# Kernel optimization log

Hardware: AMD Instinct MI355X
Metric: run time of the kernel (lower is better)

The kernel has to match this reference:

```python
import jax, jax.numpy as jnp
import numpy as np

D_MODEL = 1024
D_K = 64
MAX_LEN = 10000
SCALE = float(np.sqrt(2 * D_K))  # TUPE scale sqrt(2*d_k)


def setup_inputs() -> dict:
    key = jax.random.key(0)
    kq, kk, kv, kpe, kuq, kuk = jax.random.split(key, 6)
    b, s = 4, 2048
    q = jax.random.normal(kq, (b, s, D_MODEL), dtype=jnp.float32)
    k = jax.random.normal(kk, (b, s, D_MODEL), dtype=jnp.float32)
    v = jax.random.normal(kv, (b, s, D_MODEL), dtype=jnp.float32)
    # learned PE, uniform(-0.1, 0.1) as in the source
    pe = jax.random.uniform(kpe, (MAX_LEN, D_MODEL), minval=-0.1, maxval=0.1, dtype=jnp.float32)
    # U_q / U_k: Linear(d_model, d_model, bias=False); store as [in, out] so x @ W matches torch x @ W.T convention after transpose choice
    lim = 1.0 / np.sqrt(D_MODEL)
    Uq = jax.random.uniform(kuq, (D_MODEL, D_MODEL), minval=-lim, maxval=lim, dtype=jnp.float32)
    Uk = jax.random.uniform(kuk, (D_MODEL, D_MODEL), minval=-lim, maxval=lim, dtype=jnp.float32)
    return {"q": q, "k": k, "v": v, "pe": pe, "Uq": Uq, "Uk": Uk}


def reference(q, k, v, pe, Uq, Uk):
    b, len_q, d_model = q.shape
    len_k = k.shape[1]
    # NOTE: source computes scores with FULL q/k (over d_model), not per-head.
    scores = jnp.einsum('bqd,bkd->bqk', q, k)  # [b, lq, lk]
    # TUPE positional attention bias
    q_pe = pe[:len_q] @ Uq  # [lq, d]
    k_pe = pe[:len_k] @ Uk  # [lk, d]
    scores = scores + (q_pe @ k_pe.T)[None, :, :]
    scores = scores / SCALE
    attn = jax.nn.softmax(scores, axis=-1)  # dropout p=0 in eval
    context = jnp.einsum('bqk,bkd->bqd', attn, v)  # [b, lq, d_model]
    # replicate torch transpose(1,2).contiguous().view(b, -1, d_model)
    context = jnp.swapaxes(context, 1, 2).reshape(b, -1, d_model)
    return context, attn
```

## Files before the change

kernel.cpp:

```cpp
#include <hip/hip_runtime.h>
#include <hip/hip_bf16.h>
#include <math.h>

#define BATCH 4
#define SEQ   2048
#define DMODEL 1024

typedef __attribute__((ext_vector_type(8))) short bf16x8;
typedef __attribute__((ext_vector_type(4))) float floatx4;

__device__ __forceinline__ void async_copy16(const void* g, void* lds) {
    __builtin_amdgcn_global_load_lds(
        reinterpret_cast<const unsigned int __attribute__((address_space(1)))*>(
            reinterpret_cast<unsigned long long>(g)),
        reinterpret_cast<unsigned int __attribute__((address_space(3)))*>(
            (unsigned int)reinterpret_cast<unsigned long long>(lds)),
        16, 0, 0);
}

#define SCHED_FENCE() __builtin_amdgcn_sched_barrier(0)


#define T256(T, U, STG, RA, VMM, BARR) do {                                     \
    constexpr int sl = (U) & 3, sl1 = ((U) + 1) & 3, sl3 = ((U) + 3) & 3;       \
    constexpr int p = (U) & 1, p1 = ((U) + 1) & 1;                              \
    _Pragma("unroll") for (int i = 0; i < 4; ++i) aH[i] = readA(sl, 4 + i);     \
    if constexpr (STG) { stageA((T) + 3, 0, sl3); stageA((T) + 3, 1, sl3);      \
                         stageB((T) + 3, 0, sl3); stageB((T) + 3, 1, sl3); }    \
    asm volatile("s_waitcnt lgkmcnt(4)" ::: "memory"); SCHED_FENCE();           \
    __builtin_amdgcn_s_setprio(1);                                              \
    _Pragma("unroll") for (int i = 0; i < 4; ++i)                               \
      _Pragma("unroll") for (int j = 0; j < 4; ++j)                             \
        acc[i][j] = __builtin_amdgcn_mfma_f32_16x16x32_bf16(aP[p][i], bP[p][j], acc[i][j], 0, 0, 0); \
    __builtin_amdgcn_s_setprio(0);                                              \
    if constexpr (RA) {                                                         \
        _Pragma("unroll") for (int i = 0; i < 4; ++i) aP[p1][i] = readA(sl1, i);\
        _Pragma("unroll") for (int j = 0; j < 4; ++j) bP[p1][j] = readB(sl1, j);\
        asm volatile("s_waitcnt lgkmcnt(8)" ::: "memory");                      \
    } else {                                                                    \
        asm volatile("s_waitcnt lgkmcnt(0)" ::: "memory");                      \
    }                                                                           \
    SCHED_FENCE();                                                              \
    __builtin_amdgcn_s_setprio(1);                                              \
    _Pragma("unroll") for (int i = 0; i < 4; ++i)                               \
      _Pragma("unroll") for (int j = 0; j < 4; ++j)                             \
        acc[4 + i][j] = __builtin_amdgcn_mfma_f32_16x16x32_bf16(aH[i], bP[p][j], acc[4 + i][j], 0, 0, 0); \
    __builtin_amdgcn_s_setprio(0);                                              \
    if constexpr ((VMM) == 2)      { asm volatile("s_waitcnt vmcnt(4)" ::: "memory"); } \
    else if constexpr ((VMM) == 1) { asm volatile("s_waitcnt vmcnt(0)" ::: "memory"); } \
    if constexpr (BARR) __builtin_amdgcn_s_barrier();                           \
} while (0)

#define T128(T, U, STG, RA, VMM, BARR) do {                                     \
    constexpr int sl1 = ((U) + 1) & 3, sl3 = ((U) + 3) & 3;                     \
    constexpr int p = (U) & 1, p1 = ((U) + 1) & 1;                              \
    if constexpr (RA) {                                                         \
        _Pragma("unroll") for (int i = 0; i < 8; ++i) aP[p1][i] = readA(sl1, i);\
        _Pragma("unroll") for (int j = 0; j < 2; ++j) bP[p1][j] = readB(sl1, j);\
    }                                                                           \
    if constexpr (STG) { stageA((T) + 3, 0, sl3); stageA((T) + 3, 1, sl3);      \
                         stageB((T) + 3, 0, sl3); }                             \
    if constexpr (RA) { asm volatile("s_waitcnt lgkmcnt(10)" ::: "memory"); }   \
    else              { asm volatile("s_waitcnt lgkmcnt(0)" ::: "memory"); }    \
    SCHED_FENCE();                                                              \
    __builtin_amdgcn_s_setprio(1);                                              \
    _Pragma("unroll") for (int i = 0; i < 8; ++i)                               \
      _Pragma("unroll") for (int j = 0; j < 2; ++j)                             \
        acc[i][j] = __builtin_amdgcn_mfma_f32_16x16x32_bf16(aP[p][i], bP[p][j], acc[i][j], 0, 0, 0); \
    __builtin_amdgcn_s_setprio(0);                                              \
    if constexpr ((VMM) == 2)      { asm volatile("s_waitcnt vmcnt(3)" ::: "memory"); } \
    else if constexpr ((VMM) == 1) { asm volatile("s_waitcnt vmcnt(0)" ::: "memory"); } \
    if constexpr (BARR) __builtin_amdgcn_s_barrier();                           \
} while (0)

template<bool ASPLIT, int BN, bool HAS_BIAS, int MM, int NN, int KK, int KBB>
__global__ __launch_bounds__(512, 1)
void gemm8p(const __hip_bfloat16* __restrict__ A0, const __hip_bfloat16* __restrict__ A1,
            const __hip_bfloat16* __restrict__ B, const float* __restrict__ bias,
            float* __restrict__ C, float scale, long sAb, long sBb, long sCb)
{
    constexpr int BM = 256, BK = 32;
    constexpr int NT = KK / BK;
    constexpr int KA = ASPLIT ? (KK / 2) : KK;
    constexpr int WN = BN / 4, NF = WN / 16;
    constexpr int SLOT_A = BM * BK, SLOT_B = BN * BK;
    constexpr int GX = NN / BN, GY = MM / BM;
    constexpr int CPX = (GX * GY) / 8;
    static_assert(NT % 4 == 0 && NT >= 8, "");
    static_assert((GX * GY) % 8 == 0, "");

    __shared__ __align__(16) __hip_bfloat16 sA[4][SLOT_A];
    __shared__ __align__(16) __hip_bfloat16 sB[4][SLOT_B];

    const int bz = blockIdx.z;
    A0 += (long)bz * sAb;
    if (ASPLIT) A1 += (long)bz * sAb;
    B += (long)bz * sBb;
    C += (long)bz * sCb;

    int b = blockIdx.y * GX + blockIdx.x;
    b = (b & 7) * CPX + (b >> 3);
    const int col0 = (b % GX) * BN;
    const int row0 = (b / GX) * BM;

    const int tid  = threadIdx.x;
    const int wave = tid >> 6, lane = tid & 63;
    const int wm = wave >> 2, wn = wave & 3;
    const int fr = lane & 15, fq = lane >> 4;
    const int swz = (fq ^ ((fr >> 1) & 3)) << 3;

    const int s_r  = (wave << 4) + (lane >> 2);
    const int s_c4 = lane & 3;

    auto stageA = [&](int t, int c, int sl) {
        const int lr = (c << 7) + s_r;
        const int ch = (s_c4 ^ ((lr >> 1) & 3)) << 3;
        int k0 = t << 5;
        const __hip_bfloat16* src = A0;
        if (ASPLIT && k0 >= KA) { src = A1; k0 -= KA; }
        async_copy16(src + (long)(row0 + lr) * KA + k0 + ch,
                     &sA[sl][((c << 7) + (wave << 4)) * BK]);
    };
    auto stageB = [&](int t, int c, int sl) {
        const int lr = (c << 7) + s_r;
        const int ch = (s_c4 ^ ((lr >> 1) & 3)) << 3;
        const int k0 = (t << 5) & (KBB - 1);
        async_copy16(B + (long)(col0 + lr) * KBB + k0 + ch,
                     &sB[sl][((c << 7) + (wave << 4)) * BK]);
    };
    auto readA = [&](int sl, int i) -> bf16x8 {
        return *(const bf16x8*)&sA[sl][((wm << 7) + (i << 4) + fr) * BK + swz];
    };
    auto readB = [&](int sl, int j) -> bf16x8 {
        return *(const bf16x8*)&sB[sl][(wn * WN + (j << 4) + fr) * BK + swz];
    };

    floatx4 acc[8][NF];
    #pragma unroll
    for (int i = 0; i < 8; ++i)
        #pragma unroll
        for (int j = 0; j < NF; ++j) acc[i][j] = (floatx4){0.f, 0.f, 0.f, 0.f};

    bf16x8 aP[2][BN == 256 ? 4 : 8];
    bf16x8 bP[2][NF];
    bf16x8 aH[BN == 256 ? 4 : 1];

    if constexpr (BN == 256) {
        stageA(0, 0, 0); stageA(0, 1, 0); stageB(0, 0, 0); stageB(0, 1, 0);
        stageA(1, 0, 1); stageA(1, 1, 1); stageB(1, 0, 1); stageB(1, 1, 1);
        stageA(2, 0, 2); stageA(2, 1, 2); stageB(2, 0, 2); stageB(2, 1, 2);
        asm volatile("s_waitcnt vmcnt(4)" ::: "memory");
        __builtin_amdgcn_s_barrier(); SCHED_FENCE();
        #pragma unroll
        for (int i = 0; i < 4; ++i) aP[0][i] = readA(0, i);
        #pragma unroll
        for (int j = 0; j < 4; ++j) bP[0][j] = readB(0, j);

        #pragma unroll 1
        for (int tt = 0; tt < NT - 4; tt += 4) {
            T256(tt + 0, 0, 1, 1, 2, 1); T256(tt + 1, 1, 1, 1, 2, 1);
            T256(tt + 2, 2, 1, 1, 2, 1); T256(tt + 3, 3, 1, 1, 2, 1);
        }
        T256(NT - 4, 0, 1, 1, 2, 1);
        T256(NT - 3, 1, 0, 1, 1, 1);
        T256(NT - 2, 2, 0, 1, 0, 0);
        T256(NT - 1, 3, 0, 0, 0, 0);
    } else {
        stageA(0, 0, 0); stageA(0, 1, 0); stageB(0, 0, 0);
        stageA(1, 0, 1); stageA(1, 1, 1); stageB(1, 0, 1);
        stageA(2, 0, 2); stageA(2, 1, 2); stageB(2, 0, 2);
        asm volatile("s_waitcnt vmcnt(3)" ::: "memory");
        __builtin_amdgcn_s_barrier(); SCHED_FENCE();
        #pragma unroll
        for (int i = 0; i < 8; ++i) aP[0][i] = readA(0, i);
        #pragma unroll
        for (int j = 0; j < 2; ++j) bP[0][j] = readB(0, j);

        #pragma unroll 1
        for (int tt = 0; tt < NT - 4; tt += 4) {
            T128(tt + 0, 0, 1, 1, 2, 1); T128(tt + 1, 1, 1, 1, 2, 1);
            T128(tt + 2, 2, 1, 1, 2, 1); T128(tt + 3, 3, 1, 1, 2, 1);
        }
        T128(NT - 4, 0, 1, 1, 2, 1);
        T128(NT - 3, 1, 0, 1, 1, 1);
        T128(NT - 2, 2, 0, 1, 0, 0);
        T128(NT - 1, 3, 0, 0, 0, 0);
    }

    #pragma unroll
    for (int i = 0; i < 8; ++i) {
        #pragma unroll
        for (int r = 0; r < 4; ++r) {
            const int row = row0 + (wm << 7) + (i << 4) + (fq << 2) + r;
            #pragma unroll
            for (int j = 0; j < NF; ++j) {
                const int col = col0 + wn * WN + (j << 4) + fr;
                float val = acc[i][j][r];
                if (HAS_BIAS) val += bias[(long)row * NN + col];
                val *= scale;
                C[(long)row * NN + col] = val;
            }
        }
    }
}

template<bool SPLIT_A, bool HAS_BIAS, bool OUT_TRANS, bool OUT_BF16>
__global__ __launch_bounds__(256, 1)
void mfma_gemm(const __hip_bfloat16* __restrict__ Ah, const __hip_bfloat16* __restrict__ Al,
               const __hip_bfloat16* __restrict__ Bh,
               const float* __restrict__ bias, void* __restrict__ Cvoid,
               int M, int N, int K, float scale,
               long sAb, long sBb, long sCb)
{
    constexpr int NA = SPLIT_A ? 2 : 1;
    __shared__ __align__(16) __hip_bfloat16 sA[NA][128 * 32];
    __shared__ __align__(16) __hip_bfloat16 sB[128 * 32];

    const int bz = blockIdx.z;
    Ah += (long)bz * sAb;
    Bh += (long)bz * sBb;
    if (SPLIT_A) Al += (long)bz * sAb;

    const int row0 = blockIdx.y * 128;
    const int col0 = blockIdx.x * 128;
    const int tid  = threadIdx.x;
    const int wave = tid >> 6;
    const int lane = tid & 63;

    const int srow   = wave * 16 + (lane >> 2);
    const int schunk = (lane & 3) * 8;

    const int wm = (wave >> 1) * 64;
    const int wn = (wave & 1) * 64;
    const int fr = lane & 15;
    const int fk = (lane >> 4) * 8;

    const floatx4 zero = {0.f, 0.f, 0.f, 0.f};
    floatx4 acc[4][4];
    #pragma unroll
    for (int i = 0; i < 4; ++i)
        #pragma unroll
        for (int j = 0; j < 4; ++j) acc[i][j] = zero;

    for (int k0 = 0; k0 < K; k0 += 32) {
        #pragma unroll
        for (int t = 0; t < 2; ++t) {
            const long arow = (long)(row0 + t * 64 + srow);
            const long brow = (long)(col0 + t * 64 + srow);
            const int  soff = (t * 64 + wave * 16) * 32;
            async_copy16(Ah + arow * K + k0 + schunk, &sA[0][soff]);
            async_copy16(Bh + brow * K + k0 + schunk, &sB[soff]);
            if (SPLIT_A)
                async_copy16(Al + arow * K + k0 + schunk, &sA[NA - 1][soff]);
        }
        __syncthreads();

        bf16x8 aH[4], bH[4];
        #pragma unroll
        for (int i = 0; i < 4; ++i) aH[i] = *(const bf16x8*)&sA[0][(wm + i * 16 + fr) * 32 + fk];
        #pragma unroll
        for (int j = 0; j < 4; ++j) bH[j] = *(const bf16x8*)&sB[(wn + j * 16 + fr) * 32 + fk];

        if (SPLIT_A) {
            bf16x8 aL[4];
            #pragma unroll
            for (int i = 0; i < 4; ++i) aL[i] = *(const bf16x8*)&sA[NA - 1][(wm + i * 16 + fr) * 32 + fk];
            #pragma unroll
            for (int i = 0; i < 4; ++i)
                #pragma unroll
                for (int j = 0; j < 4; ++j) {
                    acc[i][j] = __builtin_amdgcn_mfma_f32_16x16x32_bf16(aH[i], bH[j], acc[i][j], 0, 0, 0);
                    acc[i][j] = __builtin_amdgcn_mfma_f32_16x16x32_bf16(aL[i], bH[j], acc[i][j], 0, 0, 0);
                }
        } else {
            #pragma unroll
            for (int i = 0; i < 4; ++i)
                #pragma unroll
                for (int j = 0; j < 4; ++j)
                    acc[i][j] = __builtin_amdgcn_mfma_f32_16x16x32_bf16(aH[i], bH[j], acc[i][j], 0, 0, 0);
        }
        __syncthreads();
    }

    float* Cf = (float*)Cvoid + (long)bz * sCb;
    __hip_bfloat16* Cb = (__hip_bfloat16*)Cvoid + (long)bz * sCb;
    #pragma unroll
    for (int i = 0; i < 4; ++i) {
        #pragma unroll
        for (int r = 0; r < 4; ++r) {
            const int row = row0 + wm + i * 16 + (lane >> 4) * 4 + r;
            #pragma unroll
            for (int j = 0; j < 4; ++j) {
                const int col = col0 + wn + j * 16 + (lane & 15);
                float val = acc[i][j][r];
                if (HAS_BIAS) val += bias[(long)row * N + col];
                val *= scale;
                if (OUT_BF16)       Cb[(long)row * N + col] = __float2bfloat16(val);
                else if (OUT_TRANS) Cf[(long)col * M + row] = val;
                else                Cf[(long)row * N + col] = val;
            }
        }
    }
}

__global__ __launch_bounds__(256)
void convert_bf16_kernel(const float* __restrict__ in, __hip_bfloat16* __restrict__ out, long n)
{
    const long i = ((long)blockIdx.x * 256 + threadIdx.x) * 4;
    if (i >= n) return;
    float va[4];
    *(float4*)va = *(const float4*)(in + i);
    __align__(8) __hip_bfloat16 h[4];
    #pragma unroll
    for (int j = 0; j < 4; ++j) h[j] = __float2bfloat16(va[j]);
    *(uint2*)(out + i) = *(uint2*)h;
}

__global__ __launch_bounds__(256)
void split_convert_kernel(const float* __restrict__ in, __hip_bfloat16* __restrict__ hi,
                          __hip_bfloat16* __restrict__ lo, long n)
{
    const long i = ((long)blockIdx.x * 256 + threadIdx.x) * 4;
    if (i >= n) return;
    float va[4];
    *(float4*)va = *(const float4*)(in + i);
    __align__(8) __hip_bfloat16 h[4], l[4];
    #pragma unroll
    for (int j = 0; j < 4; ++j) {
        h[j] = __float2bfloat16(va[j]);
        l[j] = __float2bfloat16(va[j] - __bfloat162float(h[j]));
    }
    *(uint2*)(hi + i) = *(uint2*)h;
    *(uint2*)(lo + i) = *(uint2*)l;
}

__global__ __launch_bounds__(256)
void transpose_convert_kernel(const float* __restrict__ in, __hip_bfloat16* __restrict__ out,
                              int R, int C, long sIn, long sOut)
{
    in  += (long)blockIdx.z * sIn;
    out += (long)blockIdx.z * sOut;
    __shared__ float t[32][33];
    const int c0 = blockIdx.x * 32, r0 = blockIdx.y * 32;
    for (int i = threadIdx.y; i < 32; i += 8)
        t[i][threadIdx.x] = in[(long)(r0 + i) * C + c0 + threadIdx.x];
    __syncthreads();
    for (int i = threadIdx.y; i < 32; i += 8)
        out[(long)(c0 + i) * R + r0 + threadIdx.x] = __float2bfloat16(t[threadIdx.x][i]);
}

__global__ __launch_bounds__(256)
void softmax_kernel(float* __restrict__ data, __hip_bfloat16* __restrict__ data_bf)
{
    const long row = blockIdx.x;
    float* p = data + row * (long)SEQ;
    __hip_bfloat16* pb = data_bf + row * (long)SEQ;
    const int tid = threadIdx.x;
    const int PER = SEQ / 256;

    float v[PER];
    float m = -1e30f;
    #pragma unroll
    for (int i = 0; i < PER; ++i) {
        v[i] = p[tid + i * 256];
        m = fmaxf(m, v[i]);
    }
    __shared__ float red[256];
    red[tid] = m;
    __syncthreads();
    #pragma unroll
    for (int s = 128; s > 0; s >>= 1) {
        if (tid < s) red[tid] = fmaxf(red[tid], red[tid + s]);
        __syncthreads();
    }
    m = red[0];
    __syncthreads();
    float sum = 0.f;
    #pragma unroll
    for (int i = 0; i < PER; ++i) {
        v[i] = __expf(v[i] - m);
        sum += v[i];
    }
    red[tid] = sum;
    __syncthreads();
    #pragma unroll
    for (int s = 128; s > 0; s >>= 1) {
        if (tid < s) red[tid] += red[tid + s];
        __syncthreads();
    }
    const float inv = 1.0f / red[0];
    #pragma unroll
    for (int i = 0; i < PER; ++i) {
        const float a = v[i] * inv;
        p[tid + i * 256]  = a;
        pb[tid + i * 256] = __float2bfloat16(a);
    }
}

extern "C" void kernel_launch(void* const* d_in, const int* in_sizes, int n_in,
                              void* d_out, int out_size, void* d_ws, size_t ws_size,
                              hipStream_t stream)
{
    const float* q  = (const float*)d_in[0];
    const float* k  = (const float*)d_in[1];
    const float* v  = (const float*)d_in[2];
    const float* pe = (const float*)d_in[3];
    const float* Uq = (const float*)d_in[4];
    const float* Uk = (const float*)d_in[5];

    float* out      = (float*)d_out;
    float* ctx_out  = out;
    float* attn_out = out + (long)BATCH * SEQ * DMODEL;

    const long SD = (long)BATCH * SEQ * DMODEL;
    char* w = (char*)d_ws;
    __hip_bfloat16* q_hi  = (__hip_bfloat16*)w;  w += SD * 2;
    __hip_bfloat16* q_lo  = (__hip_bfloat16*)w;  w += SD * 2;
    __hip_bfloat16* k_bf  = (__hip_bfloat16*)w;  w += SD * 2;
    __hip_bfloat16* pe_bf = (__hip_bfloat16*)w;  w += (long)SEQ * DMODEL * 2;
    __hip_bfloat16* UqT   = (__hip_bfloat16*)w;  w += (long)DMODEL * DMODEL * 2;
    __hip_bfloat16* UkT   = (__hip_bfloat16*)w;  w += (long)DMODEL * DMODEL * 2;
    __hip_bfloat16* qpe_bf= (__hip_bfloat16*)w;  w += (long)SEQ * DMODEL * 2;
    __hip_bfloat16* kpe_bf= (__hip_bfloat16*)w;  w += (long)SEQ * DMODEL * 2;
    float*          biasM = (float*)w;           w += (long)SEQ * SEQ * 4;
    __hip_bfloat16* attn_bf = q_hi;
    __hip_bfloat16* vT      = k_bf;

    const float inv_scale = 1.0f / sqrtf(128.0f);

    convert_bf16_kernel<<<dim3((SEQ * DMODEL) / 4 / 256), 256, 0, stream>>>(pe, pe_bf, (long)SEQ * DMODEL);
    transpose_convert_kernel<<<dim3(DMODEL / 32, DMODEL / 32, 1), dim3(32, 8), 0, stream>>>(
        Uq, UqT, DMODEL, DMODEL, 0, 0);
    transpose_convert_kernel<<<dim3(DMODEL / 32, DMODEL / 32, 1), dim3(32, 8), 0, stream>>>(
        Uk, UkT, DMODEL, DMODEL, 0, 0);
    split_convert_kernel<<<dim3(SD / 4 / 256), 256, 0, stream>>>(q, q_hi, q_lo, SD);
    convert_bf16_kernel<<<dim3(SD / 4 / 256), 256, 0, stream>>>(k, k_bf, SD);

    mfma_gemm<false, false, false, true><<<dim3(DMODEL / 128, SEQ / 128, 2), 256, 0, stream>>>(
        pe_bf, nullptr, UqT, nullptr, qpe_bf, SEQ, DMODEL, DMODEL, 1.0f,
        0, (long)DMODEL * DMODEL, (long)SEQ * DMODEL);

    mfma_gemm<false, false, false, false><<<dim3(SEQ / 128, SEQ / 128, 1), 256, 0, stream>>>(
        qpe_bf, nullptr, kpe_bf, nullptr, biasM, SEQ, SEQ, DMODEL, 1.0f, 0, 0, 0);

    gemm8p<true, 256, true, 2048, 2048, 2048, 1024>
        <<<dim3(SEQ / 256, SEQ / 256, BATCH), 512, 0, stream>>>(
        q_hi, q_lo, k_bf, biasM, attn_out, inv_scale,
        (long)SEQ * DMODEL, (long)SEQ * DMODEL, (long)SEQ * SEQ);

    softmax_kernel<<<dim3(BATCH * SEQ), 256, 0, stream>>>(attn_out, attn_bf);

    transpose_convert_kernel<<<dim3(DMODEL / 32, SEQ / 32, BATCH), dim3(32, 8), 0, stream>>>(
        v, vT, SEQ, DMODEL, (long)SEQ * DMODEL, (long)SEQ * DMODEL);

    gemm8p<false, 128, false, 1024, 2048, 2048, 2048>
        <<<dim3(SEQ / 128, DMODEL / 256, BATCH), 512, 0, stream>>>(
        vT, nullptr, attn_bf, nullptr, ctx_out, 1.0f,
        (long)SEQ * DMODEL, (long)SEQ * SEQ, (long)SEQ * DMODEL);
}
```

Measured before the change: 400.0 us.

## Retile context GEMM to 128x256, reorder staging, use shuffle softmax reductions

The context GEMM switches from a 256x128 tile to a 128x256 tile with a new 4x4 MFMA fragment layout per wave and a matching staging and wait-count schedule. In the 256-tile path, the global-to-LDS staging is moved after the first MFMA batch so it overlaps with compute. The softmax block reduction replaces the LDS tree with its many barriers by wave-level xor shuffles plus a small cross-wave combine. Together these change operand reuse and reduce synchronization, but the altered lgkmcnt/vmcnt waits must still match the new load counts.

```diff
diff --git a/kernel.cpp b/kernel.cpp
--- a/kernel.cpp
+++ b/kernel.cpp
@@ -25,14 +25,14 @@
     constexpr int sl = (U) & 3, sl1 = ((U) + 1) & 3, sl3 = ((U) + 3) & 3;       \
     constexpr int p = (U) & 1, p1 = ((U) + 1) & 1;                              \
     _Pragma("unroll") for (int i = 0; i < 4; ++i) aH[i] = readA(sl, 4 + i);     \
-    if constexpr (STG) { stageA((T) + 3, 0, sl3); stageA((T) + 3, 1, sl3);      \
-                         stageB((T) + 3, 0, sl3); stageB((T) + 3, 1, sl3); }    \
     asm volatile("s_waitcnt lgkmcnt(4)" ::: "memory"); SCHED_FENCE();           \
     __builtin_amdgcn_s_setprio(1);                                              \
     _Pragma("unroll") for (int i = 0; i < 4; ++i)                               \
       _Pragma("unroll") for (int j = 0; j < 4; ++j)                             \
         acc[i][j] = __builtin_amdgcn_mfma_f32_16x16x32_bf16(aP[p][i], bP[p][j], acc[i][j], 0, 0, 0); \
     __builtin_amdgcn_s_setprio(0);                                              \
+    if constexpr (STG) { stageA((T) + 3, 0, sl3); stageA((T) + 3, 1, sl3);      \
+                         stageB((T) + 3, 0, sl3); stageB((T) + 3, 1, sl3); }    \
     if constexpr (RA) {                                                         \
         _Pragma("unroll") for (int i = 0; i < 4; ++i) aP[p1][i] = readA(sl1, i);\
         _Pragma("unroll") for (int j = 0; j < 4; ++j) bP[p1][j] = readB(sl1, j);\
@@ -51,21 +51,21 @@
     if constexpr (BARR) __builtin_amdgcn_s_barrier();                           \
 } while (0)
 
-#define T128(T, U, STG, RA, VMM, BARR) do {                                     \
+#define TCX(T, U, STG, RA, VMM, BARR) do {                                      \
     constexpr int sl1 = ((U) + 1) & 3, sl3 = ((U) + 3) & 3;                     \
     constexpr int p = (U) & 1, p1 = ((U) + 1) & 1;                              \
     if constexpr (RA) {                                                         \
-        _Pragma("unroll") for (int i = 0; i < 8; ++i) aP[p1][i] = readA(sl1, i);\
-        _Pragma("unroll") for (int j = 0; j < 2; ++j) bP[p1][j] = readB(sl1, j);\
+        _Pragma("unroll") for (int i = 0; i < 4; ++i) aP[p1][i] = readA(sl1, i);\
+        _Pragma("unroll") for (int j = 0; j < 4; ++j) bP[p1][j] = readB(sl1, j);\
     }                                                                           \
-    if constexpr (STG) { stageA((T) + 3, 0, sl3); stageA((T) + 3, 1, sl3);      \
-                         stageB((T) + 3, 0, sl3); }                             \
-    if constexpr (RA) { asm volatile("s_waitcnt lgkmcnt(10)" ::: "memory"); }   \
+    if constexpr (STG) { stageA((T) + 3, 0, sl3);                               \
+                         stageB((T) + 3, 0, sl3); stageB((T) + 3, 1, sl3); }    \
+    if constexpr (RA) { asm volatile("s_waitcnt lgkmcnt(8)" ::: "memory"); }    \
     else              { asm volatile("s_waitcnt lgkmcnt(0)" ::: "memory"); }    \
     SCHED_FENCE();                                                              \
     __builtin_amdgcn_s_setprio(1);                                              \
-    _Pragma("unroll") for (int i = 0; i < 8; ++i)                               \
-      _Pragma("unroll") for (int j = 0; j < 2; ++j)                             \
+    _Pragma("unroll") for (int i = 0; i < 4; ++i)                               \
+      _Pragma("unroll") for (int j = 0; j < 4; ++j)                             \
         acc[i][j] = __builtin_amdgcn_mfma_f32_16x16x32_bf16(aP[p][i], bP[p][j], acc[i][j], 0, 0, 0); \
     __builtin_amdgcn_s_setprio(0);                                              \
     if constexpr ((VMM) == 2)      { asm volatile("s_waitcnt vmcnt(3)" ::: "memory"); } \
@@ -73,21 +73,24 @@
     if constexpr (BARR) __builtin_amdgcn_s_barrier();                           \
 } while (0)
 
-template<bool ASPLIT, int BN, bool HAS_BIAS, int MM, int NN, int KK, int KBB>
+template<bool ASPLIT, int BM, int BN, bool HAS_BIAS, int MM, int NN, int KK, int KBB>
 __global__ __launch_bounds__(512, 1)
 void gemm8p(const __hip_bfloat16* __restrict__ A0, const __hip_bfloat16* __restrict__ A1,
             const __hip_bfloat16* __restrict__ B, const float* __restrict__ bias,
             float* __restrict__ C, float scale, long sAb, long sBb, long sCb)
 {
-    constexpr int BM = 256, BK = 32;
+    constexpr int BK = 32;
     constexpr int NT = KK / BK;
     constexpr int KA = ASPLIT ? (KK / 2) : KK;
     constexpr int WN = BN / 4, NF = WN / 16;
+    constexpr int WM = BM / 2;
+    constexpr int MFR = WM / 16;
     constexpr int SLOT_A = BM * BK, SLOT_B = BN * BK;
     constexpr int GX = NN / BN, GY = MM / BM;
     constexpr int CPX = (GX * GY) / 8;
     static_assert(NT % 4 == 0 && NT >= 8, "");
     static_assert((GX * GY) % 8 == 0, "");
+    static_assert(BN == 256 && (BM == 256 || BM == 128), "");
 
     __shared__ __align__(16) __hip_bfloat16 sA[4][SLOT_A];
     __shared__ __align__(16) __hip_bfloat16 sB[4][SLOT_B];
@@ -129,23 +132,23 @@
                      &sB[sl][((c << 7) + (wave << 4)) * BK]);
     };
     auto readA = [&](int sl, int i) -> bf16x8 {
-        return *(const bf16x8*)&sA[sl][((wm << 7) + (i << 4) + fr) * BK + swz];
+        return *(const bf16x8*)&sA[sl][(wm * WM + (i << 4) + fr) * BK + swz];
     };
     auto readB = [&](int sl, int j) -> bf16x8 {
         return *(const bf16x8*)&sB[sl][(wn * WN + (j << 4) + fr) * BK + swz];
     };
 
-    floatx4 acc[8][NF];
-    #pragma unroll
-    for (int i = 0; i < 8; ++i)
+    floatx4 acc[MFR][NF];
+    #pragma unroll
+    for (int i = 0; i < MFR; ++i)
         #pragma unroll
         for (int j = 0; j < NF; ++j) acc[i][j] = (floatx4){0.f, 0.f, 0.f, 0.f};
 
-    bf16x8 aP[2][BN == 256 ? 4 : 8];
+    bf16x8 aP[2][4];
     bf16x8 bP[2][NF];
-    bf16x8 aH[BN == 256 ? 4 : 1];
-
-    if constexpr (BN == 256) {
+    bf16x8 aH[4];
+
+    if constexpr (BM == 256) {
         stageA(0, 0, 0); stageA(0, 1, 0); stageB(0, 0, 0); stageB(0, 1, 0);
         stageA(1, 0, 1); stageA(1, 1, 1); stageB(1, 0, 1); stageB(1, 1, 1);
         stageA(2, 0, 2); stageA(2, 1, 2); stageB(2, 0, 2); stageB(2, 1, 2);
@@ -166,32 +169,32 @@
         T256(NT - 2, 2, 0, 1, 0, 0);
         T256(NT - 1, 3, 0, 0, 0, 0);
     } else {
-        stageA(0, 0, 0); stageA(0, 1, 0); stageB(0, 0, 0);
-        stageA(1, 0, 1); stageA(1, 1, 1); stageB(1, 0, 1);
-        stageA(2, 0, 2); stageA(2, 1, 2); stageB(2, 0, 2);
+        stageA(0, 0, 0); stageB(0, 0, 0); stageB(0, 1, 0);
+        stageA(1, 0, 1); stageB(1, 0, 1); stageB(1, 1, 1);
+        stageA(2, 0, 2); stageB(2, 0, 2); stageB(2, 1, 2);
         asm volatile("s_waitcnt vmcnt(3)" ::: "memory");
         __builtin_amdgcn_s_barrier(); SCHED_FENCE();
         #pragma unroll
-        for (int i = 0; i < 8; ++i) aP[0][i] = readA(0, i);
-        #pragma unroll
-        for (int j = 0; j < 2; ++j) bP[0][j] = readB(0, j);
+        for (int i = 0; i < 4; ++i) aP[0][i] = readA(0, i);
+        #pragma unroll
+        for (int j = 0; j < 4; ++j) bP[0][j] = readB(0, j);
 
         #pragma unroll 1
         for (int tt = 0; tt < NT - 4; tt += 4) {
-            T128(tt + 0, 0, 1, 1, 2, 1); T128(tt + 1, 1, 1, 1, 2, 1);
-            T128(tt + 2, 2, 1, 1, 2, 1); T128(tt + 3, 3, 1, 1, 2, 1);
-        }
-        T128(NT - 4, 0, 1, 1, 2, 1);
-        T128(NT - 3, 1, 0, 1, 1, 1);
-        T128(NT - 2, 2, 0, 1, 0, 0);
-        T128(NT - 1, 3, 0, 0, 0, 0);
-    }
-
-    #pragma unroll
-    for (int i = 0; i < 8; ++i) {
+            TCX(tt + 0, 0, 1, 1, 2, 1); TCX(tt + 1, 1, 1, 1, 2, 1);
+            TCX(tt + 2, 2, 1, 1, 2, 1); TCX(tt + 3, 3, 1, 1, 2, 1);
+        }
+        TCX(NT - 4, 0, 1, 1, 2, 1);
+        TCX(NT - 3, 1, 0, 1, 1, 1);
+        TCX(NT - 2, 2, 0, 1, 0, 0);
+        TCX(NT - 1, 3, 0, 0, 0, 0);
+    }
+
+    #pragma unroll
+    for (int i = 0; i < MFR; ++i) {
         #pragma unroll
         for (int r = 0; r < 4; ++r) {
-            const int row = row0 + (wm << 7) + (i << 4) + (fq << 2) + r;
+            const int row = row0 + wm * WM + (i << 4) + (fq << 2) + r;
             #pragma unroll
             for (int j = 0; j < NF; ++j) {
                 const int col = col0 + wn * WN + (j << 4) + fr;
@@ -355,7 +358,8 @@
     const long row = blockIdx.x;
     float* p = data + row * (long)SEQ;
     __hip_bfloat16* pb = data_bf + row * (long)SEQ;
-    const int tid = threadIdx.x;
+    const int tid  = threadIdx.x;
+    const int lane = tid & 63, wid = tid >> 6;
     const int PER = SEQ / 256;
 
     float v[PER];
@@ -365,30 +369,25 @@
         v[i] = p[tid + i * 256];
         m = fmaxf(m, v[i]);
     }
-    __shared__ float red[256];
-    red[tid] = m;
+    #pragma unroll
+    for (int s = 32; s > 0; s >>= 1) m = fmaxf(m, __shfl_xor(m, s));
+    __shared__ float red[8];
+    if (lane == 0) red[wid] = m;
     __syncthreads();
-    #pragma unroll
-    for (int s = 128; s > 0; s >>= 1) {
-        if (tid < s) red[tid] = fmaxf(red[tid], red[tid + s]);
-        __syncthreads();
-    }
-    m = red[0];
-    __syncthreads();
+    m = fmaxf(fmaxf(red[0], red[1]), fmaxf(red[2], red[3]));
+
     float sum = 0.f;
     #pragma unroll
     for (int i = 0; i < PER; ++i) {
         v[i] = __expf(v[i] - m);
         sum += v[i];
     }
-    red[tid] = sum;
+    #pragma unroll
+    for (int s = 32; s > 0; s >>= 1) sum += __shfl_xor(sum, s);
+    if (lane == 0) red[4 + wid] = sum;
     __syncthreads();
-    #pragma unroll
-    for (int s = 128; s > 0; s >>= 1) {
-        if (tid < s) red[tid] += red[tid + s];
-        __syncthreads();
-    }
-    const float inv = 1.0f / red[0];
+    const float inv = 1.0f / (red[4] + red[5] + red[6] + red[7]);
+
     #pragma unroll
     for (int i = 0; i < PER; ++i) {
         const float a = v[i] * inv;
@@ -443,7 +442,7 @@
     mfma_gemm<false, false, false, false><<<dim3(SEQ / 128, SEQ / 128, 1), 256, 0, stream>>>(
         qpe_bf, nullptr, kpe_bf, nullptr, biasM, SEQ, SEQ, DMODEL, 1.0f, 0, 0, 0);
 
-    gemm8p<true, 256, true, 2048, 2048, 2048, 1024>
+    gemm8p<true, 256, 256, true, 2048, 2048, 2048, 1024>
         <<<dim3(SEQ / 256, SEQ / 256, BATCH), 512, 0, stream>>>(
         q_hi, q_lo, k_bf, biasM, attn_out, inv_scale,
         (long)SEQ * DMODEL, (long)SEQ * DMODEL, (long)SEQ * SEQ);
@@ -453,8 +452,8 @@
     transpose_convert_kernel<<<dim3(DMODEL / 32, SEQ / 32, BATCH), dim3(32, 8), 0, stream>>>(
         v, vT, SEQ, DMODEL, (long)SEQ * DMODEL, (long)SEQ * DMODEL);
 
-    gemm8p<false, 128, false, 1024, 2048, 2048, 2048>
-        <<<dim3(SEQ / 128, DMODEL / 256, BATCH), 512, 0, stream>>>(
+    gemm8p<false, 128, 256, false, 1024, 2048, 2048, 2048>
+        <<<dim3(SEQ / 256, DMODEL / 128, BATCH), 512, 0, stream>>>(
         vT, nullptr, attn_bf, nullptr, ctx_out, 1.0f,
         (long)SEQ * DMODEL, (long)SEQ * SEQ, (long)SEQ * DMODEL);
 }
```

Result: no change. 401.9 us (+0.5%).
